# Kernel optimization log

Hardware: AMD Instinct MI355X
Metric: run time of the kernel (lower is better)

Reference implementation:

```python
import jax, jax.numpy as jnp
import numpy as np

BETA = 0.02
TOPK = 5  # torch.topk(A, k=5) is hard-coded; forward arg k is ignored


def setup_inputs() -> dict:
    key = jax.random.key(0)
    k1, k2, k3 = jax.random.split(key, 3)
    B, Cx, C1, CA, N, D, L = 4, 16, 16, 8, 1024, 64, 64
    x = jax.random.normal(k1, (B, Cx, N, D), dtype=jnp.float32)
    A = jax.random.normal(k2, (B, CA, N, N), dtype=jnp.float32)
    mask = jax.random.uniform(k3, (B, C1, N, L), dtype=jnp.float32)
    return {"x": x, "A": A, "mask": mask, "k": 5}


def reference(x, A, mask, k):
    # x: (B,Cx,N,D), A: (B,CA,N,N), mask: (B,C1,N,L)
    # S = softmax(x @ x^T) over last dim, then mean over channel dim -> (B,1,N,N)
    S = jax.nn.softmax(jnp.einsum('bcnd,bcmd->bcnm', x, x), axis=-1)
    S = jnp.mean(S, axis=1, keepdims=True)
    # mask similarity: (B,C1,N,N)
    mm = jnp.einsum('bcnl,bcml->bcnm', mask, mask)
    mask_weight = jax.nn.sigmoid(S * mm / jnp.sqrt(jnp.float32(10.0)))
    # A averaged over its channel dim, broadcast-added -> (B,C1,N,N)
    A_out = jnp.mean(A, axis=1, keepdims=True) + BETA * mask_weight
    # top-5 neighbors per row, gather their mask rows, reduce with max
    _, idx = jax.lax.top_k(A_out, TOPK)              # (B,C1,N,5) int32
    # mask_select[b,c,i,j,l] = mask[b,c,idx[b,c,i,j],l]
    gather = jax.vmap(jax.vmap(lambda m, i: m[i]))(mask, idx)  # (B,C1,N,5,L)
    mask_updated = jnp.max(gather, axis=-2)          # (B,C1,N,L)
    return A_out, mask_updated
```

## Files before the change

### kernel.cpp

```cpp
#include <hip/hip_runtime.h>
#include <math.h>

#define NB 4
#define NCX 16
#define NC1 16
#define NCA 8
#define NN 1024
#define ND 64
#define NL 64
#define NCG 4
#define HSTRIDE 1028

typedef __attribute__((ext_vector_type(8))) short bf16x8;
typedef __attribute__((ext_vector_type(4))) float f32x4;
typedef _Float16 h4 __attribute__((ext_vector_type(4)));
typedef unsigned short u16;
typedef unsigned int u32;

__device__ __forceinline__ u16 f2b(float f) {
    u32 u = __float_as_uint(f);
    return (u16)((u + 0x7FFFu + ((u >> 16) & 1u)) >> 16);
}

__device__ __forceinline__ bf16x8 cvt8(const float* __restrict__ p) {
    float4 a = *(const float4*)p;
    float4 b = *(const float4*)(p + 4);
    bf16x8 r;
    r[0] = (short)f2b(a.x); r[1] = (short)f2b(a.y);
    r[2] = (short)f2b(a.z); r[3] = (short)f2b(a.w);
    r[4] = (short)f2b(b.x); r[5] = (short)f2b(b.y);
    r[6] = (short)f2b(b.z); r[7] = (short)f2b(b.w);
    return r;
}

__device__ __forceinline__ float sigm(float z) {
    return 1.0f / (1.0f + __expf(-z));
}

__global__ __launch_bounds__(256) void k_cvt(const float* __restrict__ src,
                                             u16* __restrict__ dst) {
    int id = blockIdx.x * 256 + threadIdx.x;
    const float4* x4 = (const float4*)src;
    float4 a = x4[2 * id];
    float4 b = x4[2 * id + 1];
    union { u16 u[8]; uint4 v; } o;
    o.u[0] = f2b(a.x); o.u[1] = f2b(a.y); o.u[2] = f2b(a.z); o.u[3] = f2b(a.w);
    o.u[4] = f2b(b.x); o.u[5] = f2b(b.y); o.u[6] = f2b(b.z); o.u[7] = f2b(b.w);
    ((uint4*)dst)[id] = o.v;
}

__global__ __launch_bounds__(256) void k_meanA(const float* __restrict__ A,
                                               float* __restrict__ meanA) {
    int id = blockIdx.x * 256 + threadIdx.x;
    int b  = id >> 18;
    int e  = id & 262143;
    const float4* A4 = (const float4*)A;
    float4 s = A4[(size_t)(b * NCA) * 262144 + e];
#pragma unroll
    for (int c = 1; c < NCA; ++c) {
        float4 v = A4[(size_t)(b * NCA + c) * 262144 + e];
        s.x += v.x; s.y += v.y; s.z += v.z; s.w += v.w;
    }
    s.x *= 0.125f; s.y *= 0.125f; s.z *= 0.125f; s.w *= 0.125f;
    ((float4*)meanA)[id] = s;
}

__global__ __launch_bounds__(512, 8) void k_smean5(const u16* __restrict__ xb,
                                                   float* __restrict__ Spart) {
    __shared__ _Float16 Lh[8 * HSTRIDE];
    const int t  = threadIdx.x;
    const int w  = t >> 6;
    const int l  = t & 63;
    const int lm = l & 15;
    const int lq = l >> 4;
    const int i0 = blockIdx.x * 8;
    const int b  = blockIdx.y;
    const int cg = blockIdx.z;
    const int rb = lq * 4;

    float mean[16];
#pragma unroll
    for (int u = 0; u < 16; ++u) mean[u] = 0.f;

    const int arow = min(i0 + lm, NN - 1);

    for (int c = cg * 4; c < cg * 4 + 4; ++c) {
        const u16* Xc = xb + (size_t)(b * NCX + c) * NN * ND;
        bf16x8 a0 = *(const bf16x8*)(Xc + arow * ND + lq * 8);
        bf16x8 a1 = *(const bf16x8*)(Xc + arow * ND + 32 + lq * 8);
#pragma unroll
        for (int tt = 0; tt < 8; ++tt) {
            int j0 = w * 128 + tt * 16;
            const u16* Bp = Xc + (j0 + lm) * ND;
            bf16x8 b0 = *(const bf16x8*)(Bp + lq * 8);
            bf16x8 b1 = *(const bf16x8*)(Bp + 32 + lq * 8);
            f32x4 acc = {0.f, 0.f, 0.f, 0.f};
            acc = __builtin_amdgcn_mfma_f32_16x16x32_bf16(a0, b0, acc, 0, 0, 0);
            acc = __builtin_amdgcn_mfma_f32_16x16x32_bf16(a1, b1, acc, 0, 0, 0);
            if (lq < 2) {
                int col = j0 + lm;
                Lh[(rb + 0) * HSTRIDE + col] = (_Float16)acc[0];
                Lh[(rb + 1) * HSTRIDE + col] = (_Float16)acc[1];
                Lh[(rb + 2) * HSTRIDE + col] = (_Float16)acc[2];
                Lh[(rb + 3) * HSTRIDE + col] = (_Float16)acc[3];
            }
        }
        __syncthreads();
        {
            const _Float16* Lp = &Lh[w * HSTRIDE];
            float v[16];
#pragma unroll
            for (int u = 0; u < 4; ++u) {
                h4 q = *(const h4*)&Lp[4 * l + 256 * u];
                v[4 * u + 0] = (float)q[0]; v[4 * u + 1] = (float)q[1];
                v[4 * u + 2] = (float)q[2]; v[4 * u + 3] = (float)q[3];
            }
            float m = v[0];
#pragma unroll
            for (int u = 1; u < 16; ++u) m = fmaxf(m, v[u]);
#pragma unroll
            for (int off = 32; off; off >>= 1) m = fmaxf(m, __shfl_xor(m, off, 64));
            float sum = 0.f;
#pragma unroll
            for (int u = 0; u < 16; ++u) { v[u] = __expf(v[u] - m); sum += v[u]; }
#pragma unroll
            for (int off = 32; off; off >>= 1) sum += __shfl_xor(sum, off, 64);
            float r = 1.0f / sum;
#pragma unroll
            for (int u = 0; u < 16; ++u) mean[u] = fmaf(v[u], r, mean[u]);
        }
        __syncthreads();
    }
    float* Sp = Spart + (((size_t)(cg * NB + b)) * NN + (i0 + w)) * NN;
#pragma unroll
    for (int u = 0; u < 4; ++u) {
        float4 o;
        o.x = mean[4 * u + 0]; o.y = mean[4 * u + 1];
        o.z = mean[4 * u + 2]; o.w = mean[4 * u + 3];
        *(float4*)(Sp + 4 * l + 256 * u) = o;
    }
}

__global__ __launch_bounds__(256) void k_sred(const float* __restrict__ Spart,
                                              float* __restrict__ Smean) {
    int id = blockIdx.x * 256 + threadIdx.x;
    int b  = id >> 18;
    int e  = id & 262143;
    const float4* P4 = (const float4*)Spart;
    float4 s = P4[(size_t)b * 262144 + e];
#pragma unroll
    for (int g = 1; g < NCG; ++g) {
        float4 v = P4[(size_t)(g * NB + b) * 262144 + e];
        s.x += v.x; s.y += v.y; s.z += v.z; s.w += v.w;
    }
    s.x *= 0.0625f; s.y *= 0.0625f; s.z *= 0.0625f; s.w *= 0.0625f;
    ((float4*)Smean)[id] = s;
}

template <bool MB>
__global__ __launch_bounds__(512, 8) void k_final5(const float* __restrict__ mask,
                                                   const u16* __restrict__ maskb,
                                                   const float* __restrict__ Smean,
                                                   const float* __restrict__ meanA,
                                                   float* __restrict__ Aout,
                                                   float* __restrict__ maskUpd) {
    __shared__ _Float16 Lh[8 * HSTRIDE];
    const int t  = threadIdx.x;
    const int w  = t >> 6;
    const int l  = t & 63;
    const int lm = l & 15;
    const int lq = l >> 4;
    const int i0 = blockIdx.x * 8;
    const int c1 = blockIdx.y;
    const int b  = blockIdx.z;
    const int rb = lq * 4;
    const int row = i0 + w;

    const float* mbase = mask + (size_t)(b * NC1 + c1) * NN * NL;
    const u16*   mbb   = maskb + (size_t)(b * NC1 + c1) * NN * NL;

    const int arow = min(i0 + lm, NN - 1);
    bf16x8 a0, a1;
    if (MB) {
        a0 = *(const bf16x8*)(mbb + arow * NL + lq * 8);
        a1 = *(const bf16x8*)(mbb + arow * NL + 32 + lq * 8);
    } else {
        a0 = cvt8(mbase + arow * NL + lq * 8);
        a1 = cvt8(mbase + arow * NL + 32 + lq * 8);
    }
#pragma unroll
    for (int tt = 0; tt < 8; ++tt) {
        int j0 = w * 128 + tt * 16;
        bf16x8 b0, b1;
        if (MB) {
            const u16* Bp = mbb + (j0 + lm) * NL;
            b0 = *(const bf16x8*)(Bp + lq * 8);
            b1 = *(const bf16x8*)(Bp + 32 + lq * 8);
        } else {
            const float* Bp = mbase + (j0 + lm) * NL;
            b0 = cvt8(Bp + lq * 8);
            b1 = cvt8(Bp + 32 + lq * 8);
        }
        f32x4 acc = {0.f, 0.f, 0.f, 0.f};
        acc = __builtin_amdgcn_mfma_f32_16x16x32_bf16(a0, b0, acc, 0, 0, 0);
        acc = __builtin_amdgcn_mfma_f32_16x16x32_bf16(a1, b1, acc, 0, 0, 0);
        if (lq < 2) {
            int col = j0 + lm;
            Lh[(rb + 0) * HSTRIDE + col] = (_Float16)acc[0];
            Lh[(rb + 1) * HSTRIDE + col] = (_Float16)acc[1];
            Lh[(rb + 2) * HSTRIDE + col] = (_Float16)acc[2];
            Lh[(rb + 3) * HSTRIDE + col] = (_Float16)acc[3];
        }
    }
    __syncthreads();

    const _Float16* Lp = &Lh[w * HSTRIDE];
    const float* Sp = Smean + ((size_t)b * NN + row) * NN;
    const float* Mp = meanA + ((size_t)b * NN + row) * NN;
    float* Ap = Aout + ((size_t)(b * NC1 + c1) * NN + row) * NN;

    float lg[16];
#pragma unroll
    for (int u = 0; u < 4; ++u) {
        int j = 4 * l + 256 * u;
        h4 q = *(const h4*)&Lp[j];
        float4 S4 = *(const float4*)(Sp + j);
        float4 M4 = *(const float4*)(Mp + j);
        float4 o;
        o.x = M4.x + 0.02f * sigm(S4.x * (float)q[0] * 0.31622776601683794f);
        o.y = M4.y + 0.02f * sigm(S4.y * (float)q[1] * 0.31622776601683794f);
        o.z = M4.z + 0.02f * sigm(S4.z * (float)q[2] * 0.31622776601683794f);
        o.w = M4.w + 0.02f * sigm(S4.w * (float)q[3] * 0.31622776601683794f);
        *(float4*)(Ap + j) = o;
        lg[4 * u + 0] = o.x; lg[4 * u + 1] = o.y;
        lg[4 * u + 2] = o.z; lg[4 * u + 3] = o.w;
    }

    int idxs[5];
#pragma unroll
    for (int p = 0; p < 5; ++p) {
        float bv = lg[0];
        int   bj = 4 * l;
#pragma unroll
        for (int k = 1; k < 16; ++k) {
            int j = 4 * l + 256 * (k >> 2) + (k & 3);
            if (lg[k] > bv) { bv = lg[k]; bj = j; }
        }
#pragma unroll
        for (int off = 32; off; off >>= 1) {
            float ov = __shfl_xor(bv, off, 64);
            int   oj = __shfl_xor(bj, off, 64);
            if (ov > bv || (ov == bv && oj < bj)) { bv = ov; bj = oj; }
        }
        idxs[p] = bj;
        const bool mine = ((bj & 255) >> 2) == l;
        const int  ck   = (bj >> 8) * 4 + (bj & 3);
#pragma unroll
        for (int k = 0; k < 16; ++k)
            lg[k] = (mine && k == ck) ? -INFINITY : lg[k];
    }
    float mx = mbase[(size_t)idxs[0] * NL + l];
#pragma unroll
    for (int p = 1; p < 5; ++p)
        mx = fmaxf(mx, mbase[(size_t)idxs[p] * NL + l]);
    maskUpd[((size_t)(b * NC1 + c1) * NN + row) * NL + l] = mx;
}

extern "C" void kernel_launch(void* const* d_in, const int* in_sizes, int n_in,
                              void* d_out, int out_size, void* d_ws, size_t ws_size,
                              hipStream_t stream) {
    const float* x    = (const float*)d_in[0];
    const float* A    = (const float*)d_in[1];
    const float* mask = (const float*)d_in[2];
    float* out     = (float*)d_out;
    float* Aout    = out;
    float* maskUpd = out + (size_t)NB * NC1 * NN * NN;
    float* meanA   = (float*)d_ws;
    float* Smean   = meanA + (size_t)NB * NN * NN;
    u16*   maskb   = (u16*)(Smean + (size_t)NB * NN * NN);
    const bool useMB = ws_size >= (size_t)(2 * NB * NN * NN * 4 + NB * NC1 * NN * NL * 2);

    u16*   xb    = (u16*)Aout;
    float* Spart = Aout + (size_t)16777216;

    hipLaunchKernelGGL(k_cvt, dim3((NB * NCX * NN * ND / 8) / 256), dim3(256), 0,
                       stream, x, xb);
    if (useMB)
        hipLaunchKernelGGL(k_cvt, dim3((NB * NC1 * NN * NL / 8) / 256), dim3(256), 0,
                           stream, mask, (u16*)maskb);
    hipLaunchKernelGGL(k_meanA, dim3((NB * NN * NN / 4) / 256), dim3(256), 0, stream,
                       A, meanA);
    hipLaunchKernelGGL(k_smean5, dim3(NN / 8, NB, NCG), dim3(512), 0, stream,
                       xb, Spart);
    hipLaunchKernelGGL(k_sred, dim3((NB * NN * NN / 4) / 256), dim3(256), 0, stream,
                       Spart, Smean);
    if (useMB)
        hipLaunchKernelGGL(k_final5<true>, dim3(NN / 8, NC1, NB), dim3(512), 0,
                           stream, mask, maskb, Smean, meanA, Aout, maskUpd);
    else
        hipLaunchKernelGGL(k_final5<false>, dim3(NN / 8, NC1, NB), dim3(512), 0,
                           stream, mask, maskb, Smean, meanA, Aout, maskUpd);
}
```

Before: 679.4 us.

## Precompute top-5 threshold from mean A and use all MFMA rows in smean

A new kernel computes, for each row of the channel-averaged A, the fifth-largest value as a threshold. The final kernel counts the A_out entries at or above that threshold with wave ballots. When exactly five qualify, it gathers their mask rows directly and skips the serial five-pass top-k reduction; otherwise it falls back to the old selection. Separately, the softmax-mean kernel now processes 16 rows per block so all four MFMA output quads are stored and used instead of discarding half. This costs an extra pass over meanA, a larger LDS footprint that lowers the occupancy hint, and different tie handling when the fast path is taken.

New measurement: 639.0 us. 5.9% less time.

```diff
diff --git a/kernel.cpp b/kernel.cpp
--- a/kernel.cpp
+++ b/kernel.cpp
@@ -16,6 +16,7 @@
 typedef _Float16 h4 __attribute__((ext_vector_type(4)));
 typedef unsigned short u16;
 typedef unsigned int u32;
+typedef unsigned long long u64;
 
 __device__ __forceinline__ u16 f2b(float f) {
     u32 u = __float_as_uint(f);
@@ -65,24 +66,65 @@
     ((float4*)meanA)[id] = s;
 }
 
-__global__ __launch_bounds__(512, 8) void k_smean5(const u16* __restrict__ xb,
+__global__ __launch_bounds__(512) void k_thresh(const float* __restrict__ meanA,
+                                                float* __restrict__ T) {
+    const int t = threadIdx.x;
+    const int w = t >> 6;
+    const int l = t & 63;
+    const int row = blockIdx.x * 8 + w;
+    const float* Mp = meanA + (size_t)row * NN;
+    float v[16];
+#pragma unroll
+    for (int u = 0; u < 4; ++u) {
+        float4 q = *(const float4*)(Mp + 4 * l + 256 * u);
+        v[4 * u + 0] = q.x; v[4 * u + 1] = q.y;
+        v[4 * u + 2] = q.z; v[4 * u + 3] = q.w;
+    }
+    float bv = 0.f;
+#pragma unroll
+    for (int p = 0; p < 5; ++p) {
+        bv = v[0];
+        int bj = 4 * l;
+#pragma unroll
+        for (int k = 1; k < 16; ++k) {
+            int j = 4 * l + 256 * (k >> 2) + (k & 3);
+            if (v[k] > bv) { bv = v[k]; bj = j; }
+        }
+#pragma unroll
+        for (int off = 32; off; off >>= 1) {
+            float ov = __shfl_xor(bv, off, 64);
+            int   oj = __shfl_xor(bj, off, 64);
+            if (ov > bv || (ov == bv && oj < bj)) { bv = ov; bj = oj; }
+        }
+        const bool mine = ((bj & 255) >> 2) == l;
+        const int  ck   = (bj >> 8) * 4 + (bj & 3);
+#pragma unroll
+        for (int k = 0; k < 16; ++k)
+            v[k] = (mine && k == ck) ? -INFINITY : v[k];
+    }
+    if (l == 0) T[row] = bv;
+}
+
+__global__ __launch_bounds__(512, 6) void k_smean6(const u16* __restrict__ xb,
                                                    float* __restrict__ Spart) {
-    __shared__ _Float16 Lh[8 * HSTRIDE];
+    __shared__ _Float16 Lh[16 * HSTRIDE];
     const int t  = threadIdx.x;
     const int w  = t >> 6;
     const int l  = t & 63;
     const int lm = l & 15;
     const int lq = l >> 4;
-    const int i0 = blockIdx.x * 8;
+    const int i0 = blockIdx.x * 16;
     const int b  = blockIdx.y;
     const int cg = blockIdx.z;
     const int rb = lq * 4;
 
-    float mean[16];
-#pragma unroll
-    for (int u = 0; u < 16; ++u) mean[u] = 0.f;
-
-    const int arow = min(i0 + lm, NN - 1);
+    float mean[2][16];
+#pragma unroll
+    for (int s = 0; s < 2; ++s)
+#pragma unroll
+        for (int u = 0; u < 16; ++u) mean[s][u] = 0.f;
+
+    const int arow = i0 + lm;
 
     for (int c = cg * 4; c < cg * 4 + 4; ++c) {
         const u16* Xc = xb + (size_t)(b * NCX + c) * NN * ND;
@@ -97,17 +139,16 @@
             f32x4 acc = {0.f, 0.f, 0.f, 0.f};
             acc = __builtin_amdgcn_mfma_f32_16x16x32_bf16(a0, b0, acc, 0, 0, 0);
             acc = __builtin_amdgcn_mfma_f32_16x16x32_bf16(a1, b1, acc, 0, 0, 0);
-            if (lq < 2) {
-                int col = j0 + lm;
-                Lh[(rb + 0) * HSTRIDE + col] = (_Float16)acc[0];
-                Lh[(rb + 1) * HSTRIDE + col] = (_Float16)acc[1];
-                Lh[(rb + 2) * HSTRIDE + col] = (_Float16)acc[2];
-                Lh[(rb + 3) * HSTRIDE + col] = (_Float16)acc[3];
-            }
+            int col = j0 + lm;
+            Lh[(rb + 0) * HSTRIDE + col] = (_Float16)acc[0];
+            Lh[(rb + 1) * HSTRIDE + col] = (_Float16)acc[1];
+            Lh[(rb + 2) * HSTRIDE + col] = (_Float16)acc[2];
+            Lh[(rb + 3) * HSTRIDE + col] = (_Float16)acc[3];
         }
         __syncthreads();
-        {
-            const _Float16* Lp = &Lh[w * HSTRIDE];
+#pragma unroll
+        for (int s = 0; s < 2; ++s) {
+            const _Float16* Lp = &Lh[(2 * w + s) * HSTRIDE];
             float v[16];
 #pragma unroll
             for (int u = 0; u < 4; ++u) {
@@ -127,17 +168,20 @@
             for (int off = 32; off; off >>= 1) sum += __shfl_xor(sum, off, 64);
             float r = 1.0f / sum;
 #pragma unroll
-            for (int u = 0; u < 16; ++u) mean[u] = fmaf(v[u], r, mean[u]);
+            for (int u = 0; u < 16; ++u) mean[s][u] = fmaf(v[u], r, mean[s][u]);
         }
         __syncthreads();
     }
-    float* Sp = Spart + (((size_t)(cg * NB + b)) * NN + (i0 + w)) * NN;
-#pragma unroll
-    for (int u = 0; u < 4; ++u) {
-        float4 o;
-        o.x = mean[4 * u + 0]; o.y = mean[4 * u + 1];
-        o.z = mean[4 * u + 2]; o.w = mean[4 * u + 3];
-        *(float4*)(Sp + 4 * l + 256 * u) = o;
+#pragma unroll
+    for (int s = 0; s < 2; ++s) {
+        float* Sp = Spart + (((size_t)(cg * NB + b)) * NN + (i0 + 2 * w + s)) * NN;
+#pragma unroll
+        for (int u = 0; u < 4; ++u) {
+            float4 o;
+            o.x = mean[s][4 * u + 0]; o.y = mean[s][4 * u + 1];
+            o.z = mean[s][4 * u + 2]; o.w = mean[s][4 * u + 3];
+            *(float4*)(Sp + 4 * l + 256 * u) = o;
+        }
     }
 }
 
@@ -157,11 +201,12 @@
     ((float4*)Smean)[id] = s;
 }
 
-template <bool MB>
-__global__ __launch_bounds__(512, 8) void k_final5(const float* __restrict__ mask,
+template <bool FAST>
+__global__ __launch_bounds__(512, 8) void k_final6(const float* __restrict__ mask,
                                                    const u16* __restrict__ maskb,
                                                    const float* __restrict__ Smean,
                                                    const float* __restrict__ meanA,
+                                                   const float* __restrict__ T,
                                                    float* __restrict__ Aout,
                                                    float* __restrict__ maskUpd) {
     __shared__ _Float16 Lh[8 * HSTRIDE];
@@ -181,7 +226,7 @@
 
     const int arow = min(i0 + lm, NN - 1);
     bf16x8 a0, a1;
-    if (MB) {
+    if (FAST) {
         a0 = *(const bf16x8*)(mbb + arow * NL + lq * 8);
         a1 = *(const bf16x8*)(mbb + arow * NL + 32 + lq * 8);
     } else {
@@ -192,7 +237,7 @@
     for (int tt = 0; tt < 8; ++tt) {
         int j0 = w * 128 + tt * 16;
         bf16x8 b0, b1;
-        if (MB) {
+        if (FAST) {
             const u16* Bp = mbb + (j0 + lm) * NL;
             b0 = *(const bf16x8*)(Bp + lq * 8);
             b1 = *(const bf16x8*)(Bp + 32 + lq * 8);
@@ -236,33 +281,57 @@
         lg[4 * u + 2] = o.z; lg[4 * u + 3] = o.w;
     }
 
-    int idxs[5];
-#pragma unroll
-    for (int p = 0; p < 5; ++p) {
-        float bv = lg[0];
-        int   bj = 4 * l;
-#pragma unroll
-        for (int k = 1; k < 16; ++k) {
-            int j = 4 * l + 256 * (k >> 2) + (k & 3);
-            if (lg[k] > bv) { bv = lg[k]; bj = j; }
-        }
-#pragma unroll
-        for (int off = 32; off; off >>= 1) {
-            float ov = __shfl_xor(bv, off, 64);
-            int   oj = __shfl_xor(bj, off, 64);
-            if (ov > bv || (ov == bv && oj < bj)) { bv = ov; bj = oj; }
-        }
-        idxs[p] = bj;
-        const bool mine = ((bj & 255) >> 2) == l;
-        const int  ck   = (bj >> 8) * 4 + (bj & 3);
+    float mx = -INFINITY;
+    bool done = false;
+    if (FAST) {
+        const float Tr = T[(size_t)b * NN + row];
+        int m = 0;
 #pragma unroll
         for (int k = 0; k < 16; ++k)
-            lg[k] = (mine && k == ck) ? -INFINITY : lg[k];
-    }
-    float mx = mbase[(size_t)idxs[0] * NL + l];
-#pragma unroll
-    for (int p = 1; p < 5; ++p)
-        mx = fmaxf(mx, mbase[(size_t)idxs[p] * NL + l]);
+            m += __popcll(__ballot(lg[k] >= Tr));
+        if (m == 5) {
+#pragma unroll
+            for (int k = 0; k < 16; ++k) {
+                u64 bk = __ballot(lg[k] >= Tr);
+                while (bk) {
+                    int src = __ffsll((unsigned long long)bk) - 1;
+                    bk &= bk - 1;
+                    int idx = 4 * src + 256 * (k >> 2) + (k & 3);
+                    mx = fmaxf(mx, mbase[(size_t)idx * NL + l]);
+                }
+            }
+            done = true;
+        }
+    }
+    if (!done) {
+        int idxs[5];
+#pragma unroll
+        for (int p = 0; p < 5; ++p) {
+            float bv = lg[0];
+            int   bj = 4 * l;
+#pragma unroll
+            for (int k = 1; k < 16; ++k) {
+                int j = 4 * l + 256 * (k >> 2) + (k & 3);
+                if (lg[k] > bv) { bv = lg[k]; bj = j; }
+            }
+#pragma unroll
+            for (int off = 32; off; off >>= 1) {
+                float ov = __shfl_xor(bv, off, 64);
+                int   oj = __shfl_xor(bj, off, 64);
+                if (ov > bv || (ov == bv && oj < bj)) { bv = ov; bj = oj; }
+            }
+            idxs[p] = bj;
+            const bool mine = ((bj & 255) >> 2) == l;
+            const int  ck   = (bj >> 8) * 4 + (bj & 3);
+#pragma unroll
+            for (int k = 0; k < 16; ++k)
+                lg[k] = (mine && k == ck) ? -INFINITY : lg[k];
+        }
+        mx = mbase[(size_t)idxs[0] * NL + l];
+#pragma unroll
+        for (int p = 1; p < 5; ++p)
+            mx = fmaxf(mx, mbase[(size_t)idxs[p] * NL + l]);
+    }
     maskUpd[((size_t)(b * NC1 + c1) * NN + row) * NL + l] = mx;
 }
 
@@ -278,26 +347,33 @@
     float* meanA   = (float*)d_ws;
     float* Smean   = meanA + (size_t)NB * NN * NN;
     u16*   maskb   = (u16*)(Smean + (size_t)NB * NN * NN);
-    const bool useMB = ws_size >= (size_t)(2 * NB * NN * NN * 4 + NB * NC1 * NN * NL * 2);
+    float* T       = (float*)(maskb + (size_t)NB * NC1 * NN * NL);
+    const size_t need = (size_t)2 * NB * NN * NN * 4
+                      + (size_t)NB * NC1 * NN * NL * 2
+                      + (size_t)NB * NN * 4;
+    const bool fast = ws_size >= need;
 
     u16*   xb    = (u16*)Aout;
     float* Spart = Aout + (size_t)16777216;
 
     hipLaunchKernelGGL(k_cvt, dim3((NB * NCX * NN * ND / 8) / 256), dim3(256), 0,
                        stream, x, xb);
-    if (useMB)
+    if (fast)
         hipLaunchKernelGGL(k_cvt, dim3((NB * NC1 * NN * NL / 8) / 256), dim3(256), 0,
                            stream, mask, (u16*)maskb);
     hipLaunchKernelGGL(k_meanA, dim3((NB * NN * NN / 4) / 256), dim3(256), 0, stream,
                        A, meanA);
-    hipLaunchKernelGGL(k_smean5, dim3(NN / 8, NB, NCG), dim3(512), 0, stream,
+    if (fast)
+        hipLaunchKernelGGL(k_thresh, dim3(NB * NN / 8), dim3(512), 0, stream,
+                           meanA, T);
+    hipLaunchKernelGGL(k_smean6, dim3(NN / 16, NB, NCG), dim3(512), 0, stream,
                        xb, Spart);
     hipLaunchKernelGGL(k_sred, dim3((NB * NN * NN / 4) / 256), dim3(256), 0, stream,
                        Spart, Smean);
-    if (useMB)
-        hipLaunchKernelGGL(k_final5<true>, dim3(NN / 8, NC1, NB), dim3(512), 0,
-                           stream, mask, maskb, Smean, meanA, Aout, maskUpd);
+    if (fast)
+        hipLaunchKernelGGL(k_final6<true>, dim3(NN / 8, NC1, NB), dim3(512), 0,
+                           stream, mask, maskb, Smean, meanA, T, Aout, maskUpd);
     else
-        hipLaunchKernelGGL(k_final5<false>, dim3(NN / 8, NC1, NB), dim3(512), 0,
-                           stream, mask, maskb, Smean, meanA, Aout, maskUpd);
-}
+        hipLaunchKernelGGL(k_final6<false>, dim3(NN / 8, NC1, NB), dim3(512), 0,
+                           stream, mask, maskb, Smean, meanA, T, Aout, maskUpd);
+}
```
